# Kernel optimization log

Measured on AMD Instinct MI355X. Metric: run time of the kernel, lower is better.

Reference implementation:

```python
import math
import jax, jax.numpy as jnp
import numpy as np

B, T, I, H = 32, 64, 256, 512
TAU = 20.0                      # tau_trace and membrane tau
DECAY = math.exp(-1.0 / TAU)    # exp trace decay (exp_convolve)
ALPHA = math.exp(-1.0 / TAU)    # leaky-integrator membrane decay
ETA = 0.1                       # Hebbian plasticity learning rate


def setup_inputs() -> dict:
    key = jax.random.key(0)
    kx, kw = jax.random.split(key)
    x = jax.random.normal(kx, (B, T, I), dtype=jnp.float32)
    # xavier_uniform with gain sqrt(2) ~ normal with matched std
    std = math.sqrt(2.0) * math.sqrt(2.0 / (2 * H + I))
    W = (jax.random.normal(kw, (2 * H, I), dtype=jnp.float32) * std)
    return {"x": x, "W": W}


def reference(x, W):
    """Write-mode (recall=False) forward of MemoryLayer.
    Returns (mem [B,H,H], keys [B,T,H], vals [B,T,H])."""
    h = W.shape[0] // 2
    b = x.shape[0]
    # i = linear(x, W): [B,T,2H], split into key/value drives
    i = jnp.einsum('bti,hi->bth', x, W)
    ik, iv = i[..., :h], i[..., h:]

    mem0 = jnp.zeros((b, h, h), x.dtype)
    z = jnp.zeros((b, h), x.dtype)

    def step(carry, inp):
        kv, vv, kt, vt, mem = carry
        ik_t, iv_t = inp
        # key neuron dynamics: leaky integration + tanh
        kv = ALPHA * kv + ik_t
        k = jnp.tanh(kv)
        # associative read: (key.unsqueeze(1) * mem).sum(2) == mem @ key
        ikv = 0.2 * jnp.einsum('bij,bj->bi', mem, k)
        # value neuron dynamics
        vv = ALPHA * vv + iv_t + ikv
        v = jnp.tanh(vv)
        # exp_convolve traces
        kt = DECAY * kt + (1.0 - DECAY) * k
        vt = DECAY * vt + (1.0 - DECAY) * v
        # Hebbian outer-product plasticity: delta_mem = eta * vt (x) kt
        mem = mem + ETA * jnp.einsum('bi,bj->bij', vt, kt)
        return (kv, vv, kt, vt, mem), (k, v)

    # scan over time (sequential recurrence), batch fully vectorized
    (kv, vv, kt, vt, mem), (ks, vs) = jax.lax.scan(
        step, (z, z, z, z, mem0),
        (jnp.swapaxes(ik, 0, 1), jnp.swapaxes(iv, 0, 1)))
    keys = jnp.swapaxes(ks, 0, 1)  # [B,T,H]
    vals = jnp.swapaxes(vs, 0, 1)  # [B,T,H]
    return mem, keys, vals
```

## Files before the change

kernel.cpp:

```cpp
#include <hip/hip_runtime.h>

#define B_ 32
#define T_ 64
#define I_ 256
#define H_ 512

static constexpr float ALPHA_F = 0.951229424500714f;
static constexpr float OMD_F   = 0.048770575499286f;
static constexpr float ETA_F   = 0.1f;
static constexpr float CSCALE  = 0.02f;

typedef __bf16 bf16x8 __attribute__((ext_vector_type(8)));
typedef float  f32x4  __attribute__((ext_vector_type(4)));

__device__ __forceinline__ float tanh_fast(float x) {
  float xc = fminf(fmaxf(x, -15.f), 15.f);
  float e = __expf(2.f * xc);
  return (e - 1.f) * __builtin_amdgcn_rcpf(e + 1.f);
}
__device__ __forceinline__ unsigned int f2bf(float f) {
  unsigned int u = __float_as_uint(f);
  u += 0x7fffu + ((u >> 16) & 1u);
  return u >> 16;
}

template <int CTRL>
__device__ __forceinline__ float dpp_add(float x) {
  int mv = __builtin_amdgcn_update_dpp(0, __float_as_int(x), CTRL, 0xF, 0xF, true);
  return x + __int_as_float(mv);
}
__device__ __forceinline__ float wave_sum_dpp(float x) {
  x = dpp_add<0x111>(x);
  x = dpp_add<0x112>(x);
  x = dpp_add<0x114>(x);
  x = dpp_add<0x118>(x);
  x = dpp_add<0x142>(x);
  x = dpp_add<0x143>(x);
  return x;
}

__global__ __launch_bounds__(256) void proj_kscan(const float* __restrict__ x,
                                                  const float* __restrict__ W,
                                                  float* __restrict__ keys,
                                                  float* __restrict__ ktg,
                                                  ushort* __restrict__ ktb16T,
                                                  float* __restrict__ ivbuf) {
  __shared__ float Ak[64][68];
  __shared__ float Bk[64][68];
  const int b  = blockIdx.x;
  const int n0 = blockIdx.y * 64;
  const int m0 = b * 64;
  const int tid = threadIdx.x;
  const int ty = tid >> 4, tx = tid & 15;
  const int sr = tid >> 2;
  const int sc = tid & 3;
  float acc[4][4] = {};

  for (int k0 = 0; k0 < I_; k0 += 64) {
#pragma unroll
    for (int e = 0; e < 4; ++e) {
      const int cq = sc + 4 * e;
      float4 xv = *reinterpret_cast<const float4*>(&x[(size_t)(m0 + sr) * I_ + k0 + cq * 4]);
      Ak[cq * 4 + 0][sr] = xv.x;
      Ak[cq * 4 + 1][sr] = xv.y;
      Ak[cq * 4 + 2][sr] = xv.z;
      Ak[cq * 4 + 3][sr] = xv.w;
      float4 wv = *reinterpret_cast<const float4*>(&W[(size_t)(n0 + sr) * I_ + k0 + cq * 4]);
      Bk[cq * 4 + 0][sr] = wv.x;
      Bk[cq * 4 + 1][sr] = wv.y;
      Bk[cq * 4 + 2][sr] = wv.z;
      Bk[cq * 4 + 3][sr] = wv.w;
    }
    __syncthreads();
#pragma unroll 8
    for (int kk = 0; kk < 64; ++kk) {
      float4 a4 = *reinterpret_cast<const float4*>(&Ak[kk][ty * 4]);
      float4 b4 = *reinterpret_cast<const float4*>(&Bk[kk][tx * 4]);
      float av[4] = {a4.x, a4.y, a4.z, a4.w};
      float bv[4] = {b4.x, b4.y, b4.z, b4.w};
#pragma unroll
      for (int i = 0; i < 4; ++i)
#pragma unroll
        for (int j = 0; j < 4; ++j) acc[i][j] += av[i] * bv[j];
    }
    __syncthreads();
  }

  if (n0 < 512) {
    float* scr = &Ak[0][0];
#pragma unroll
    for (int i = 0; i < 4; ++i)
#pragma unroll
      for (int j = 0; j < 4; ++j) scr[(ty * 4 + i) * 68 + tx * 4 + j] = acc[i][j];
    __syncthreads();
    if (tid < 64) {
      float kv = 0.f, kt = 0.f;
      unsigned int kpk[32];
      float* ko  = keys + (size_t)b * T_ * H_ + n0 + tid;
      float* kto = ktg  + (size_t)b * T_ * H_ + n0 + tid;
#pragma unroll
      for (int t = 0; t < T_; ++t) {
        kv = ALPHA_F * kv + scr[t * 68 + tid];
        float k = tanh_fast(kv);
        kt = ALPHA_F * kt + OMD_F * k;
        ko[(size_t)t * H_]  = k;
        kto[(size_t)t * H_] = kt;
        unsigned int us = f2bf(kt);
        if ((t & 1) == 0) kpk[t >> 1] = us;
        else              kpk[t >> 1] |= us << 16;
      }
      ushort* kb = ktb16T + ((size_t)b * H_ + n0 + tid) * T_;
#pragma unroll
      for (int e = 0; e < 8; ++e)
        reinterpret_cast<uint4*>(kb)[e] =
            make_uint4(kpk[4 * e], kpk[4 * e + 1], kpk[4 * e + 2], kpk[4 * e + 3]);
    }
  } else {
    const int hv0 = n0 - 512;
#pragma unroll
    for (int i = 0; i < 4; ++i)
      *reinterpret_cast<float4*>(&ivbuf[((size_t)b * T_ + ty * 4 + i) * H_ + hv0 + tx * 4]) =
          make_float4(acc[i][0], acc[i][1], acc[i][2], acc[i][3]);
  }
}

__global__ __launch_bounds__(512) void dots_kernel(const float* __restrict__ keys,
                                                   const float* __restrict__ ktg,
                                                   float* __restrict__ C) {
  const int b = blockIdx.y;
  const int t = blockIdx.x * 8 + (threadIdx.x >> 6);
  const int lane = threadIdx.x & 63;
  const float* krow = keys + ((size_t)b * T_ + t) * H_ + 4 * lane;
  float4 k0 = *reinterpret_cast<const float4*>(krow);
  float4 k1 = *reinterpret_cast<const float4*>(krow + 256);
  const float* tb = ktg + (size_t)b * T_ * H_ + 4 * lane;
  float* Cb = C + ((size_t)b * T_ + t) * T_;
#pragma unroll 8
  for (int s = 0; s < T_; ++s) {
    const float* ar = tb + (size_t)s * H_;
    float4 a0 = *reinterpret_cast<const float4*>(ar);
    float4 a1 = *reinterpret_cast<const float4*>(ar + 256);
    float p = a0.x * k0.x + a0.y * k0.y + a0.z * k0.z + a0.w * k0.w
            + a1.x * k1.x + a1.y * k1.y + a1.z * k1.z + a1.w * k1.w;
    p = wave_sum_dpp(p);
    if (lane == 63) Cb[s] = CSCALE * p;
  }
}

#define IVG(T) (((T) & 3) == 0 ? ivq[(T) >> 2].x : ((T) & 3) == 1 ? ivq[(T) >> 2].y \
              : ((T) & 3) == 2 ? ivq[(T) >> 2].z : ivq[(T) >> 2].w)
#define VQSET(T, val) do { \
    if (((T) & 3) == 0)      vqv[(T) >> 2].x = (val); \
    else if (((T) & 3) == 1) vqv[(T) >> 2].y = (val); \
    else if (((T) & 3) == 2) vqv[(T) >> 2].z = (val); \
    else                     vqv[(T) >> 2].w = (val); } while (0)

#define VSTEP(TT, CUR, NXT)                                                   \
  {                                                                           \
    if ((TT) + 1 < T_) {                                                      \
      _Pragma("unroll")                                                       \
      for (int q = 0; q < 16; ++q)                                            \
        NXT[q] = *reinterpret_cast<const float4*>(&Cs[(TT) + 1][4 * q]);      \
    }                                                                         \
    float p0 = 0.f, p1 = 0.f, p2 = 0.f, p3 = 0.f;                             \
    _Pragma("unroll")                                                         \
    for (int q = 0; q < 16; ++q) {                                            \
      p0 += CUR[q].x * vqv[q].x;                                              \
      p1 += CUR[q].y * vqv[q].y;                                              \
      p2 += CUR[q].z * vqv[q].z;                                              \
      p3 += CUR[q].w * vqv[q].w;                                              \
    }                                                                         \
    float ikv = (p0 + p1) + (p2 + p3);                                        \
    vv = ALPHA_F * vv + IVG(TT) + ikv;                                        \
    float v = tanh_fast(vv);                                                  \
    vt = ALPHA_F * vt + OMD_F * v;                                            \
    VQSET(TT, vt);                                                            \
    vo[(size_t)(TT) * H_] = v;                                                \
  }

#define VP2(T2) VSTEP(T2, ca, cbuf) VSTEP((T2) + 1, cbuf, ca)
#define VP8(T8) VP2(T8) VP2((T8) + 2) VP2((T8) + 4) VP2((T8) + 6)
#define IVLD(Q) { ivq[Q].x = pv[(size_t)(4 * (Q) + 0) * H_]; \
                  ivq[Q].y = pv[(size_t)(4 * (Q) + 1) * H_]; \
                  ivq[Q].z = pv[(size_t)(4 * (Q) + 2) * H_]; \
                  ivq[Q].w = pv[(size_t)(4 * (Q) + 3) * H_]; }

__global__ __launch_bounds__(64, 1) void vscan_kernel(const float* __restrict__ ivbuf,
                                                      const float* __restrict__ C,
                                                      float* __restrict__ vals,
                                                      ushort* __restrict__ vtb16T) {
  __shared__ float Cs[T_][T_];
  const int b    = blockIdx.x >> 3;
  const int lane = threadIdx.x;
  const int h    = ((blockIdx.x & 7) << 6) + lane;

  const float* Cb = C + (size_t)b * T_ * T_;
#pragma unroll
  for (int e = 0; e < 16; ++e)
    reinterpret_cast<float4*>(&Cs[0][0])[lane + (e << 6)] =
        reinterpret_cast<const float4*>(Cb)[lane + (e << 6)];

  const float* pv = ivbuf + (size_t)b * T_ * H_ + h;
  float* vo = vals + ((size_t)b * T_) * H_ + h;

  float4 ivq[16];
  IVLD(0)  IVLD(1)  IVLD(2)  IVLD(3)  IVLD(4)  IVLD(5)  IVLD(6)  IVLD(7)
  IVLD(8)  IVLD(9)  IVLD(10) IVLD(11) IVLD(12) IVLD(13) IVLD(14) IVLD(15)

  float vv = 0.f, vt = 0.f;
  float4 vqv[16];
#pragma unroll
  for (int q = 0; q < 16; ++q) vqv[q] = make_float4(0.f, 0.f, 0.f, 0.f);

  __syncthreads();

  float4 ca[16], cbuf[16];
#pragma unroll
  for (int q = 0; q < 16; ++q)
    ca[q] = *reinterpret_cast<const float4*>(&Cs[0][4 * q]);

  VP8(0) VP8(8) VP8(16) VP8(24) VP8(32) VP8(40) VP8(48) VP8(56)

  ushort* vb16 = vtb16T + ((size_t)b * H_ + h) * T_;
#pragma unroll
  for (int q = 0; q < 16; ++q) {
    unsigned int u0 = f2bf(vqv[q].x) | (f2bf(vqv[q].y) << 16);
    unsigned int u1 = f2bf(vqv[q].z) | (f2bf(vqv[q].w) << 16);
    reinterpret_cast<uint2*>(vb16)[q] = make_uint2(u0, u1);
  }
}

__global__ __launch_bounds__(256) void mem_mfma(const ushort* __restrict__ vtb16T,
                                                const ushort* __restrict__ ktb16T,
                                                float* __restrict__ mem) {
  const int b  = blockIdx.z;
  const int i0 = blockIdx.y * 64;
  const int j0 = blockIdx.x * 64;
  const int tid = threadIdx.x;
  const int w = tid >> 6, l = tid & 63;
  const int lrow = l & 15, lk8 = (l >> 4) * 8;

  const ushort* ar = vtb16T + ((size_t)b * H_ + i0 + w * 16 + lrow) * T_ + lk8;
  const ushort* br = ktb16T + ((size_t)b * H_ + j0 + lrow) * T_ + lk8;
  f32x4 acc[4] = {};
#pragma unroll
  for (int ks = 0; ks < 2; ++ks) {
    bf16x8 a = *reinterpret_cast<const bf16x8*>(ar + ks * 32);
#pragma unroll
    for (int jt = 0; jt < 4; ++jt) {
      bf16x8 bv = *reinterpret_cast<const bf16x8*>(br + (size_t)jt * 16 * T_ + ks * 32);
      acc[jt] = __builtin_amdgcn_mfma_f32_16x16x32_bf16(a, bv, acc[jt], 0, 0, 0);
    }
  }
  const int tr0 = (l >> 4) * 4, tc = lrow;
  float* mb = mem + (size_t)b * H_ * H_;
#pragma unroll
  for (int jt = 0; jt < 4; ++jt)
#pragma unroll
    for (int r = 0; r < 4; ++r)
      mb[((size_t)i0 + w * 16 + tr0 + r) * H_ + j0 + jt * 16 + tc] = ETA_F * acc[jt][r];
}

extern "C" void kernel_launch(void* const* d_in, const int* in_sizes, int n_in,
                              void* d_out, int out_size, void* d_ws, size_t ws_size,
                              hipStream_t stream) {
  const float* x = (const float*)d_in[0];
  const float* W = (const float*)d_in[1];
  float* out = (float*)d_out;
  float* mem  = out;
  float* keys = out + (size_t)B_ * H_ * H_;
  float* vals = keys + (size_t)B_ * T_ * H_;

  float*  ktg    = (float*)d_ws;
  float*  ivbuf  = ktg + (size_t)B_ * T_ * H_;
  ushort* ktb16T = (ushort*)(ivbuf + (size_t)B_ * T_ * H_);
  ushort* vtb16T = ktb16T + (size_t)B_ * H_ * T_;
  float*  Cbuf   = (float*)(vtb16T + (size_t)B_ * H_ * T_);

  proj_kscan<<<dim3(B_, 16), 256, 0, stream>>>(x, W, keys, ktg, ktb16T, ivbuf);
  dots_kernel<<<dim3(8, B_), 512, 0, stream>>>(keys, ktg, Cbuf);
  vscan_kernel<<<dim3(8 * B_), 64, 0, stream>>>(ivbuf, Cbuf, vals, vtb16T);
  mem_mfma<<<dim3(8, 8, B_), 256, 0, stream>>>(vtb16T, ktb16T, mem);
}
```

Measured before the change: 90.36 us.

## Compute input projection with split-bf16 MFMA instead of scalar FMA tiles

Replaces the LDS-tiled fp32 scalar GEMM in the projection kernel with bf16 MFMA 16x16x32 instructions. Each fp32 operand is split into hi and lo bf16 parts and three products are accumulated to approximate fp32 accuracy. Operands are loaded straight from global memory per lane with no shared-memory staging. The aim is to speed up the projection part of the pipeline, at the cost of slightly lower precision and uncoalesced, redundant global loads of W across waves.

Result: slower. 94.75 us (+4.9%).

```diff
diff --git a/kernel.cpp b/kernel.cpp
--- a/kernel.cpp
+++ b/kernel.cpp
@@ -22,6 +22,17 @@
   unsigned int u = __float_as_uint(f);
   u += 0x7fffu + ((u >> 16) & 1u);
   return u >> 16;
+}
+__device__ __forceinline__ void split8(const float* p, bf16x8& hi, bf16x8& lo) {
+  float4 f0 = *reinterpret_cast<const float4*>(p);
+  float4 f1 = *reinterpret_cast<const float4*>(p + 4);
+  float f[8] = {f0.x, f0.y, f0.z, f0.w, f1.x, f1.y, f1.z, f1.w};
+#pragma unroll
+  for (int i = 0; i < 8; ++i) {
+    __bf16 h = (__bf16)f[i];
+    hi[i] = h;
+    lo[i] = (__bf16)(f[i] - (float)h);
+  }
 }
 
 template <int CTRL>
@@ -45,53 +56,38 @@
                                                   float* __restrict__ ktg,
                                                   ushort* __restrict__ ktb16T,
                                                   float* __restrict__ ivbuf) {
-  __shared__ float Ak[64][68];
-  __shared__ float Bk[64][68];
+  __shared__ float scr[64][68];
   const int b  = blockIdx.x;
   const int n0 = blockIdx.y * 64;
   const int m0 = b * 64;
   const int tid = threadIdx.x;
-  const int ty = tid >> 4, tx = tid & 15;
-  const int sr = tid >> 2;
-  const int sc = tid & 3;
-  float acc[4][4] = {};
-
-  for (int k0 = 0; k0 < I_; k0 += 64) {
-#pragma unroll
-    for (int e = 0; e < 4; ++e) {
-      const int cq = sc + 4 * e;
-      float4 xv = *reinterpret_cast<const float4*>(&x[(size_t)(m0 + sr) * I_ + k0 + cq * 4]);
-      Ak[cq * 4 + 0][sr] = xv.x;
-      Ak[cq * 4 + 1][sr] = xv.y;
-      Ak[cq * 4 + 2][sr] = xv.z;
-      Ak[cq * 4 + 3][sr] = xv.w;
-      float4 wv = *reinterpret_cast<const float4*>(&W[(size_t)(n0 + sr) * I_ + k0 + cq * 4]);
-      Bk[cq * 4 + 0][sr] = wv.x;
-      Bk[cq * 4 + 1][sr] = wv.y;
-      Bk[cq * 4 + 2][sr] = wv.z;
-      Bk[cq * 4 + 3][sr] = wv.w;
+  const int w = tid >> 6, l = tid & 63;
+  const int lrow = l & 15, lk8 = (l >> 4) * 8;
+
+  const float* xr = x + (size_t)(m0 + w * 16 + lrow) * I_ + lk8;
+  const float* wr = W + (size_t)(n0 + lrow) * I_ + lk8;
+  f32x4 acc[4] = {};
+#pragma unroll
+  for (int ks = 0; ks < 8; ++ks) {
+    bf16x8 ah, al;
+    split8(xr + ks * 32, ah, al);
+#pragma unroll
+    for (int jt = 0; jt < 4; ++jt) {
+      bf16x8 bh, bl;
+      split8(wr + (size_t)jt * 16 * I_ + ks * 32, bh, bl);
+      acc[jt] = __builtin_amdgcn_mfma_f32_16x16x32_bf16(ah, bh, acc[jt], 0, 0, 0);
+      acc[jt] = __builtin_amdgcn_mfma_f32_16x16x32_bf16(al, bh, acc[jt], 0, 0, 0);
+      acc[jt] = __builtin_amdgcn_mfma_f32_16x16x32_bf16(ah, bl, acc[jt], 0, 0, 0);
     }
-    __syncthreads();
-#pragma unroll 8
-    for (int kk = 0; kk < 64; ++kk) {
-      float4 a4 = *reinterpret_cast<const float4*>(&Ak[kk][ty * 4]);
-      float4 b4 = *reinterpret_cast<const float4*>(&Bk[kk][tx * 4]);
-      float av[4] = {a4.x, a4.y, a4.z, a4.w};
-      float bv[4] = {b4.x, b4.y, b4.z, b4.w};
-#pragma unroll
-      for (int i = 0; i < 4; ++i)
-#pragma unroll
-        for (int j = 0; j < 4; ++j) acc[i][j] += av[i] * bv[j];
-    }
-    __syncthreads();
-  }
+  }
+  const int tr0 = (l >> 4) * 4, tc = lrow;
 
   if (n0 < 512) {
-    float* scr = &Ak[0][0];
-#pragma unroll
-    for (int i = 0; i < 4; ++i)
-#pragma unroll
-      for (int j = 0; j < 4; ++j) scr[(ty * 4 + i) * 68 + tx * 4 + j] = acc[i][j];
+#pragma unroll
+    for (int jt = 0; jt < 4; ++jt)
+#pragma unroll
+      for (int r = 0; r < 4; ++r)
+        scr[w * 16 + tr0 + r][jt * 16 + tc] = acc[jt][r];
     __syncthreads();
     if (tid < 64) {
       float kv = 0.f, kt = 0.f;
@@ -100,7 +96,7 @@
       float* kto = ktg  + (size_t)b * T_ * H_ + n0 + tid;
 #pragma unroll
       for (int t = 0; t < T_; ++t) {
-        kv = ALPHA_F * kv + scr[t * 68 + tid];
+        kv = ALPHA_F * kv + scr[t][tid];
         float k = tanh_fast(kv);
         kt = ALPHA_F * kt + OMD_F * k;
         ko[(size_t)t * H_]  = k;
@@ -118,9 +114,10 @@
   } else {
     const int hv0 = n0 - 512;
 #pragma unroll
-    for (int i = 0; i < 4; ++i)
-      *reinterpret_cast<float4*>(&ivbuf[((size_t)b * T_ + ty * 4 + i) * H_ + hv0 + tx * 4]) =
-          make_float4(acc[i][0], acc[i][1], acc[i][2], acc[i][3]);
+    for (int jt = 0; jt < 4; ++jt)
+#pragma unroll
+      for (int r = 0; r < 4; ++r)
+        ivbuf[((size_t)b * T_ + w * 16 + tr0 + r) * H_ + hv0 + jt * 16 + tc] = acc[jt][r];
   }
 }
 
```
